# Performance work log

Measured on AMD Instinct MI355X. Metric: run time of the kernel, lower is better.

The kernel has to match this reference:

```python
import jax, jax.numpy as jnp
import numpy as np

T, HID, H, KV, D = 2048, 2048, 16, 8, 128
EPS = 1e-6
THETA = 10000.0


def setup_inputs() -> dict:
    key = jax.random.key(0)
    ks = jax.random.split(key, 6)
    positions = jnp.arange(T, dtype=jnp.int64 if jax.config.jax_enable_x64 else jnp.int32)
    hidden_states = jax.random.normal(ks[0], (T, HID), dtype=jnp.float32)
    scale = 0.02
    Wq = jax.random.normal(ks[1], (HID, H * 2 * D), dtype=jnp.float32) * scale
    Wk = jax.random.normal(ks[2], (HID, KV * D), dtype=jnp.float32) * scale
    Wv = jax.random.normal(ks[3], (HID, KV * D), dtype=jnp.float32) * scale
    Wo = jax.random.normal(ks[4], (H * D, HID), dtype=jnp.float32) * scale
    q_norm_w = jnp.zeros((D,), dtype=jnp.float32)  # torch init: zeros, applied as (1+w)
    k_norm_w = jnp.zeros((D,), dtype=jnp.float32)
    return {"positions": positions, "hidden_states": hidden_states, "Wq": Wq,
            "Wk": Wk, "Wv": Wv, "Wo": Wo, "q_norm_w": q_norm_w, "k_norm_w": k_norm_w}


def _rms_norm(x, w):
    # fp32 RMSNorm with (1 + weight) scaling, per last dim
    xf = x.astype(jnp.float32)
    inv = jax.lax.rsqrt(jnp.mean(xf * xf, axis=-1, keepdims=True) + EPS)
    return (xf * inv * (1.0 + w.astype(jnp.float32))).astype(x.dtype)


def _rope(x, positions):
    # neox-style rotary over full head_dim; x: (T, heads, D)
    half = D // 2
    inv_freq = 1.0 / (THETA ** (jnp.arange(0, half, dtype=jnp.float32) / half))
    freqs = positions.astype(jnp.float32)[:, None] * inv_freq  # (T, half)
    cos = jnp.cos(freqs)[:, None, :]  # (T,1,half)
    sin = jnp.sin(freqs)[:, None, :]
    x1, x2 = x[..., :half], x[..., half:]
    return jnp.concatenate([x1 * cos - x2 * sin, x2 * cos + x1 * sin], axis=-1)


def reference(positions, hidden_states, Wq, Wk, Wv, Wo, q_norm_w, k_norm_w):
    scaling = D ** -0.5
    qg = (hidden_states @ Wq).reshape(T, H, 2 * D)
    q, gate = qg[..., :D], qg[..., D:]              # (T,H,D) each
    k = (hidden_states @ Wk).reshape(T, KV, D)
    v = (hidden_states @ Wv).reshape(T, KV, D)
    q = _rms_norm(q, q_norm_w)
    k = _rms_norm(k, k_norm_w)
    q = _rope(q, positions)
    k = _rope(k, positions)
    # GQA: repeat kv heads
    rep = H // KV
    k = jnp.repeat(k, rep, axis=1)                   # (T,H,D)
    v = jnp.repeat(v, rep, axis=1)
    scores = jnp.einsum('thd,shd->hts', q, k) * scaling  # (H,T,T)
    causal = positions[:, None] >= positions[None, :]     # (T,T)
    scores = jnp.where(causal[None], scores, jnp.finfo(scores.dtype).min)
    probs = jax.nn.softmax(scores, axis=-1)
    o = jnp.einsum('hts,shd->thd', probs, v).reshape(T, H * D)
    o = o * jax.nn.sigmoid(gate.reshape(T, H * D))
    return o @ Wo
```

## Files before the change

kernel.cpp:

```cpp
#include <hip/hip_runtime.h>
#include <stdint.h>
#include <math.h>

#define T_SEQ 2048
#define HID   2048
#define NH    16
#define NKV   8
#define DH    128

typedef __bf16 bf16x8 __attribute__((ext_vector_type(8)));
typedef float  f32x4  __attribute__((ext_vector_type(4)));

__device__ __forceinline__ ushort f2bf(float f) {
  uint32_t u = __float_as_uint(f);
  u += 0x7FFF + ((u >> 16) & 1);
  return (ushort)(u >> 16);
}
__device__ __forceinline__ ushort f2bf_rz(float f) {
  return (ushort)(__float_as_uint(f) >> 16);
}
__device__ __forceinline__ float bf2f(ushort u) {
  return __uint_as_float(((uint32_t)u) << 16);
}
__device__ __forceinline__ void gld16(const void* g, void* l) {
  __builtin_amdgcn_global_load_lds(
      (const __attribute__((address_space(1))) uint32_t*)g,
      (__attribute__((address_space(3))) uint32_t*)l, 16, 0, 0);
}

__global__ __launch_bounds__(256) void prep_kernel(
    const float* __restrict__ hs, const float* __restrict__ Wq,
    const float* __restrict__ Wk, const float* __restrict__ Wv,
    const float* __restrict__ Wo, ushort* __restrict__ hs16,
    ushort* __restrict__ Wqt, ushort* __restrict__ Wkt,
    ushort* __restrict__ Wvt, ushort* __restrict__ Wot) {
  int bid = blockIdx.x;
  if (bid < 4096) {
    int i = (bid * 256 + threadIdx.x) * 4;
    float4 v = *(const float4*)(hs + i);
    ushort4 o = {f2bf(v.x), f2bf(v.y), f2bf(v.z), f2bf(v.w)};
    *(ushort4*)(hs16 + i) = o;
    return;
  }
  bid -= 4096;
  const float* src; ushort* dst; int N, bi, bj;
  if (bid < 2048)      { src = Wq; dst = Wqt; N = 4096; bj = bid & 63; bi = bid >> 6; }
  else if (bid < 2560) { bid -= 2048; src = Wk; dst = Wkt; N = 1024; bj = bid & 15; bi = bid >> 4; }
  else if (bid < 3072) { bid -= 2560; src = Wv; dst = Wvt; N = 1024; bj = bid & 15; bi = bid >> 4; }
  else                 { bid -= 3072; src = Wo; dst = Wot; N = 2048; bj = bid & 31; bi = bid >> 5; }
  __shared__ float tile[64][65];
  const int r = threadIdx.x >> 2, cg = (threadIdx.x & 3) * 16;
  const float* sp = src + (size_t)(bi * 64 + r) * N + bj * 64 + cg;
#pragma unroll
  for (int p = 0; p < 4; ++p) {
    float4 v = *(const float4*)(sp + p * 4);
    tile[r][cg + p * 4 + 0] = v.x; tile[r][cg + p * 4 + 1] = v.y;
    tile[r][cg + p * 4 + 2] = v.z; tile[r][cg + p * 4 + 3] = v.w;
  }
  __syncthreads();
  ushort* dp = dst + (size_t)(bj * 64 + r) * HID + bi * 64 + cg;
#pragma unroll
  for (int p = 0; p < 2; ++p) {
    union { uint4 v; ushort u[8]; } o;
#pragma unroll
    for (int j = 0; j < 8; ++j) o.u[j] = f2bf(tile[cg + p * 8 + j][r]);
    *(uint4*)(dp + p * 8) = o.v;
  }
}

template <int MI>
__device__ __forceinline__ void gemm_loop(
    const ushort* __restrict__ A, const ushort* __restrict__ Bt,
    int K, int m0, int n0, ushort* As, ushort* Bs, f32x4 (*acc)[4]) {
  const int tid = threadIdx.x, lane = tid & 63, w = tid >> 6;
  const int quad = lane >> 4, l15 = lane & 15;
  const int wm = (w >> 1) * (MI * 16), wn = (w & 1) * 64;
  const int srow = tid >> 2, sch = tid & 3;
  for (int k0 = 0; k0 < K; k0 += 32) {
    __syncthreads();
#pragma unroll
    for (int p = 0; p < MI / 2; ++p) {
      int row = p * 64 + srow;
      int gch = sch ^ ((row >> 1) & 3);
      gld16(A + (size_t)(m0 + row) * K + k0 + gch * 8,
            As + (p * 256 + w * 64) * 8);
    }
#pragma unroll
    for (int p = 0; p < 2; ++p) {
      int row = p * 64 + srow;
      int gch = sch ^ ((row >> 1) & 3);
      gld16(Bt + (size_t)(n0 + row) * K + k0 + gch * 8,
            Bs + (p * 256 + w * 64) * 8);
    }
    __syncthreads();
    bf16x8 af[MI], bfr[4];
#pragma unroll
    for (int mi = 0; mi < MI; ++mi) {
      int row = wm + mi * 16 + l15;
      int pch = quad ^ ((row >> 1) & 3);
      af[mi] = *(const bf16x8*)(As + row * 32 + pch * 8);
    }
#pragma unroll
    for (int ni = 0; ni < 4; ++ni) {
      int row = wn + ni * 16 + l15;
      int pch = quad ^ ((row >> 1) & 3);
      bfr[ni] = *(const bf16x8*)(Bs + row * 32 + pch * 8);
    }
#pragma unroll
    for (int mi = 0; mi < MI; ++mi)
#pragma unroll
      for (int ni = 0; ni < 4; ++ni)
        acc[mi][ni] = __builtin_amdgcn_mfma_f32_16x16x32_bf16(
            af[mi], bfr[ni], acc[mi][ni], 0, 0, 0);
  }
}


__device__ __forceinline__ void stage_half(const ushort* __restrict__ X,
                                           int Ksrc, int rowg0, int k0,
                                           ushort* lbase) {
  const int tid = threadIdx.x;
  const int rl = tid >> 3, ch = tid & 7, w = tid >> 6;
  const int gch = ch ^ (rl & 7);
#pragma unroll
  for (int p = 0; p < 2; ++p)
    gld16(X + (size_t)(rowg0 + p * 64 + rl) * Ksrc + k0 + gch * 8,
          lbase + p * 4096 + w * 512);
}

__device__ __forceinline__ void load_a(const ushort* base, int wr, int quad,
                                       int l15, bf16x8 af[4][2]) {
  const int sw = l15 & 7;
#pragma unroll
  for (int mi = 0; mi < 4; ++mi) {
    const ushort* rp = base + (wr * 64 + mi * 16 + l15) * 64;
#pragma unroll
    for (int ks = 0; ks < 2; ++ks)
      af[mi][ks] = *(const bf16x8*)(rp + ((ks * 4 + quad) ^ sw) * 8);
  }
}
__device__ __forceinline__ void load_b(const ushort* base, int wc, int quad,
                                       int l15, bf16x8 bq[2][2]) {
  const int sw = l15 & 7;
#pragma unroll
  for (int ni = 0; ni < 2; ++ni) {
    const ushort* rp = base + (wc * 32 + ni * 16 + l15) * 64;
#pragma unroll
    for (int ks = 0; ks < 2; ++ks)
      bq[ni][ks] = *(const bf16x8*)(rp + ((ks * 4 + quad) ^ sw) * 8);
  }
}
__device__ __forceinline__ void mfma_quad(const bf16x8 af[4][2],
                                          const bf16x8 bq[2][2],
                                          f32x4 acc[8][4], int mh, int nh) {
#pragma unroll
  for (int ks = 0; ks < 2; ++ks)
#pragma unroll
    for (int mi = 0; mi < 4; ++mi)
#pragma unroll
      for (int ni = 0; ni < 2; ++ni)
        acc[mh * 4 + mi][nh * 2 + ni] =
            __builtin_amdgcn_mfma_f32_16x16x32_bf16(
                af[mi][ks], bq[ni][ks], acc[mh * 4 + mi][nh * 2 + ni], 0, 0, 0);
}

#define PHASE_MID()                                     \
  __builtin_amdgcn_s_barrier();                         \
  asm volatile("s_waitcnt lgkmcnt(0)" ::: "memory");    \
  __builtin_amdgcn_sched_barrier(0)

__global__ __launch_bounds__(512, 2) void gemm_qkv256(
    const ushort* __restrict__ hs16, const ushort* __restrict__ Wqt,
    const ushort* __restrict__ Wkt, const ushort* __restrict__ Wvt,
    ushort* __restrict__ q16, ushort* __restrict__ gate16,
    ushort* __restrict__ k16, ushort* __restrict__ v16t) {
  __shared__ ushort As[2][2][8192];
  __shared__ ushort Bs[2][2][8192];

  const int b = blockIdx.x;
  const ushort* A; const ushort* Bt; int m0, n0, kind;
  if (b < 128)      { A = hs16; Bt = Wqt; m0 = (b >> 4) << 8; n0 = (b & 15) << 8; kind = 0; }
  else if (b < 160) { int f = b - 128; A = hs16; Bt = Wkt; m0 = (f >> 2) << 8; n0 = (f & 3) << 8; kind = 1; }
  else              { int f = b - 160; A = Wvt; Bt = hs16; m0 = (f >> 3) << 8; n0 = (f & 7) << 8; kind = 2; }

  const int tid = threadIdx.x, lane = tid & 63;
  const int quad = lane >> 4, l15 = lane & 15;
  const int wid = tid >> 6, wr = wid >> 2, wc = wid & 3;

  f32x4 acc[8][4];
#pragma unroll
  for (int i = 0; i < 8; ++i)
#pragma unroll
    for (int j = 0; j < 4; ++j) acc[i][j] = (f32x4){0.f, 0.f, 0.f, 0.f};

  constexpr int K = HID;
  constexpr int NKT = K / 64;

  stage_half(A,  K, m0,        0, &As[0][0][0]);
  stage_half(A,  K, m0 + 128,  0, &As[0][1][0]);
  stage_half(Bt, K, n0,        0, &Bs[0][0][0]);
  stage_half(Bt, K, n0 + 128,  0, &Bs[0][1][0]);
  stage_half(A,  K, m0,       64, &As[1][0][0]);
  stage_half(Bt, K, n0 + 128, 64, &Bs[1][1][0]);
  asm volatile("s_waitcnt vmcnt(4)" ::: "memory");
  __builtin_amdgcn_s_barrier();

  bf16x8 af[4][2], bq0[2][2], bq1[2][2];

#pragma unroll 1
  for (int t = 0; t < NKT; ++t) {
    const int buf = t & 1, nbuf = buf ^ 1;
    const ushort* pA0 = &As[buf][0][0];
    const ushort* pA1 = &As[buf][1][0];
    const ushort* pB0 = &Bs[buf][0][0];
    const ushort* pB1 = &Bs[buf][1][0];
    const int kt1 = (t + 1) * 64, kt2 = (t + 2) * 64;

    load_a(pA0, wr, quad, l15, af);
    load_b(pB0, wc, quad, l15, bq0);
    if (t + 1 < NKT) stage_half(Bt, K, n0, kt1, &Bs[nbuf][0][0]);
    PHASE_MID();
    __builtin_amdgcn_s_setprio(1);
    mfma_quad(af, bq0, acc, 0, 0);
    __builtin_amdgcn_s_setprio(0);
    __builtin_amdgcn_s_barrier();

    load_b(pB1, wc, quad, l15, bq1);
    if (t + 1 < NKT) stage_half(A, K, m0 + 128, kt1, &As[nbuf][1][0]);
    PHASE_MID();
    __builtin_amdgcn_s_setprio(1);
    mfma_quad(af, bq1, acc, 0, 1);
    __builtin_amdgcn_s_setprio(0);
    __builtin_amdgcn_s_barrier();

    load_a(pA1, wr, quad, l15, af);
    if (t + 2 < NKT) stage_half(A, K, m0, kt2, &As[buf][0][0]);
    PHASE_MID();
    __builtin_amdgcn_s_setprio(1);
    mfma_quad(af, bq1, acc, 1, 1);
    __builtin_amdgcn_s_setprio(0);
    __builtin_amdgcn_s_barrier();

    load_b(pB0, wc, quad, l15, bq0);
    if (t + 2 < NKT) stage_half(Bt, K, n0 + 128, kt2, &Bs[buf][1][0]);
    PHASE_MID();
    __builtin_amdgcn_s_setprio(1);
    mfma_quad(af, bq0, acc, 1, 0);
    __builtin_amdgcn_s_setprio(0);
    if (t + 2 < NKT) asm volatile("s_waitcnt vmcnt(4)" ::: "memory");
    else             asm volatile("s_waitcnt vmcnt(0)" ::: "memory");
    __builtin_amdgcn_s_barrier();
  }

  const int head = n0 >> 8;
#pragma unroll
  for (int mh = 0; mh < 2; ++mh)
#pragma unroll
    for (int mi = 0; mi < 4; ++mi)
#pragma unroll
      for (int nh = 0; nh < 2; ++nh)
#pragma unroll
        for (int ni = 0; ni < 2; ++ni)
#pragma unroll
          for (int r = 0; r < 4; ++r) {
            const int row = m0 + mh * 128 + wr * 64 + mi * 16 + quad * 4 + r;
            const int ic = wc * 32 + ni * 16 + l15;
            const ushort v = f2bf(acc[mh * 4 + mi][nh * 2 + ni][r]);
            if (kind == 0) {
              ushort* dst = nh ? gate16 : q16;
              dst[((size_t)row * NH + head) * DH + ic] = v;
            } else if (kind == 1) {
              k16[(size_t)row * 1024 + n0 + nh * 128 + ic] = v;
            } else {
              v16t[(size_t)row * T_SEQ + n0 + nh * 128 + ic] = v;
            }
          }
}

__global__ __launch_bounds__(256) void gemm_out(
    const ushort* __restrict__ ob16, const ushort* __restrict__ Wot,
    float* __restrict__ out) {
  __shared__ ushort As[64 * 32];
  __shared__ ushort Bs[128 * 32];
  f32x4 acc[2][4];
#pragma unroll
  for (int i = 0; i < 2; ++i)
#pragma unroll
    for (int j = 0; j < 4; ++j) acc[i][j] = (f32x4){0.f, 0.f, 0.f, 0.f};
  const int b = blockIdx.x;
  const int m0 = (b >> 4) * 64, n0 = (b & 15) * 128;
  gemm_loop<2>(ob16, Wot, HID, m0, n0, As, Bs, acc);
  const int lane = threadIdx.x & 63, w = threadIdx.x >> 6;
  const int quad = lane >> 4, l15 = lane & 15;
  const int wm = (w >> 1) * 32, wn = (w & 1) * 64;
#pragma unroll
  for (int mi = 0; mi < 2; ++mi)
#pragma unroll
    for (int ni = 0; ni < 4; ++ni)
#pragma unroll
      for (int r = 0; r < 4; ++r) {
        int row = m0 + wm + mi * 16 + quad * 4 + r;
        int col = n0 + wn + ni * 16 + l15;
        out[(size_t)row * HID + col] = acc[mi][ni][r];
      }
}

__global__ __launch_bounds__(128) void norm_qk(
    ushort* __restrict__ q16, ushort* __restrict__ k16,
    const int* __restrict__ positions, const float* __restrict__ qw,
    const float* __restrict__ kw) {
  const int t = blockIdx.x, hh = blockIdx.y, d = threadIdx.x;
  ushort* x; const float* wgt;
  if (hh < NH) { x = q16 + ((size_t)t * NH + hh) * DH; wgt = qw; }
  else         { x = k16 + ((size_t)t * NKV + (hh - NH)) * DH; wgt = kw; }
  float v = bf2f(x[d]);
  float ss = v * v;
#pragma unroll
  for (int off = 32; off >= 1; off >>= 1) ss += __shfl_xor(ss, off, 64);
  __shared__ float red[2];
  if ((d & 63) == 0) red[d >> 6] = ss;
  __syncthreads();
  float mean = (red[0] + red[1]) * (1.0f / 128.0f);
  float xn = v * rsqrtf(mean + 1e-6f) * (1.0f + wgt[d]);
  __shared__ float sh[128];
  sh[d] = xn;
  __syncthreads();
  if (d < 64) {
    float pos = (float)positions[t];
    float rev = pos * exp2f((float)d * -0.20762050593045233f) *
                0.15915494309189535f;
    float fr = rev - floorf(rev);
    float s = __builtin_amdgcn_sinf(fr);
    float c = __builtin_amdgcn_cosf(fr);
    float x1 = sh[d], x2 = sh[d + 64];
    x[d]      = f2bf(x1 * c - x2 * s);
    x[d + 64] = f2bf(x2 * c + x1 * s);
  }
}

__global__ __launch_bounds__(256) void attn_mfma(
    const ushort* __restrict__ q16, const ushort* __restrict__ k16,
    const ushort* __restrict__ v16t, const float* __restrict__ qnw,
    const float* __restrict__ knw, ushort* __restrict__ Op0,
    ushort* __restrict__ Op1, ushort* __restrict__ Op2,
    float* __restrict__ lpart) {
  const int pb = blockIdx.x, h = blockIdx.y, s = blockIdx.z, kvh = h >> 1;
  const int tid = threadIdx.x, lane = tid & 63, w = tid >> 6;
  const int quad = lane >> 4, l15 = lane & 15;

  __shared__ ushort Ks[64 * 128];
  __shared__ ushort Vs[144 * 64];
  __shared__ ushort Ps[4][16][72];

  for (int i = tid; i < 16 * 64; i += 256) {
    int row = 128 + (i >> 6), col = i & 63;
    Vs[row * 64 + col] = (row == 128) ? (ushort)0x3F80 : (ushort)0;
  }

  __shared__ float s8[8];
  __shared__ float bshare;
  {
    float mq = 0.f, mk = 0.f;
    if (tid < 128) { mq = fabsf(1.f + qnw[tid]); mk = fabsf(1.f + knw[tid]); }
#pragma unroll
    for (int off = 32; off >= 1; off >>= 1) {
      mq = fmaxf(mq, __shfl_xor(mq, off, 64));
      mk = fmaxf(mk, __shfl_xor(mk, off, 64));
    }
    if (lane == 0) { s8[w * 2] = mq; s8[w * 2 + 1] = mk; }
    __syncthreads();
    if (tid == 0) {
      float MQ = fmaxf(s8[0], s8[2]), MK = fmaxf(s8[1], s8[3]);
      bshare = 16.3217f * MQ * MK * 1.02f + 0.1f;
    }
    __syncthreads();
  }
  const float B = bshare;
  const float CSC = 0.08838834764831845f * 1.44269504088896f;

#pragma unroll 1
  for (int sel = 0; sel < 2; ++sel) {
    const int qt = sel ? (31 - pb) : pb;
    const int q0 = qt * 64;
    const int ntl = (qt >= s) ? ((qt - s) / 3 + 1) : 0;

    bf16x8 qf[4];
    const ushort* qbase = q16 + ((size_t)(q0 + w * 16 + l15) * NH + h) * DH;
#pragma unroll
    for (int ks = 0; ks < 4; ++ks)
      qf[ks] = *(const bf16x8*)(qbase + ks * 32 + quad * 8);

    f32x4 oacc[9];
#pragma unroll
    for (int i = 0; i < 9; ++i) oacc[i] = (f32x4){0.f, 0.f, 0.f, 0.f};

#pragma unroll 1
    for (int it = 0; it < ntl; ++it) {
      const int kt = s + 3 * it;
      const int kt0 = kt * 64;
      __syncthreads();
#pragma unroll
      for (int p = 0; p < 4; ++p) {
        int row = p * 16 + (tid >> 4), ch = tid & 15;
        int gch = ch ^ (row & 15);
        gld16(k16 + ((size_t)(kt0 + row) * NKV + kvh) * DH + gch * 8,
              Ks + (p * 256 + w * 64) * 8);
      }
#pragma unroll
      for (int p = 0; p < 4; ++p) {
        int row = p * 32 + (tid >> 3), ch = tid & 7;
        int gch = ch ^ (row & 7);
        gld16(v16t + (size_t)(kvh * DH + row) * T_SEQ + kt0 + gch * 8,
              Vs + (p * 256 + w * 64) * 8);
      }
      __syncthreads();

      f32x4 sacc[4];
#pragma unroll
      for (int ni = 0; ni < 4; ++ni) sacc[ni] = (f32x4){0.f, 0.f, 0.f, 0.f};
#pragma unroll
      for (int ks = 0; ks < 4; ++ks)
#pragma unroll
        for (int ni = 0; ni < 4; ++ni) {
          int row = ni * 16 + l15;
          int pch = (ks * 4 + quad) ^ (row & 15);
          bf16x8 kf = *(const bf16x8*)(Ks + row * 128 + pch * 8);
          sacc[ni] = __builtin_amdgcn_mfma_f32_16x16x32_bf16(
              qf[ks], kf, sacc[ni], 0, 0, 0);
        }

      const bool diag = (kt == qt);
#pragma unroll
      for (int ni = 0; ni < 4; ++ni) {
        int key = kt0 + ni * 16 + l15;
#pragma unroll
        for (int r = 0; r < 4; ++r) {
          float arg = fmaf(sacc[ni][r], CSC, -B);
          float pv;
          if (diag) {
            int q = q0 + w * 16 + quad * 4 + r;
            pv = (key <= q) ? exp2f(arg) : 0.f;
          } else {
            pv = exp2f(arg);
          }
          Ps[w][quad * 4 + r][ni * 16 + l15] = f2bf_rz(pv);
        }
      }

#pragma unroll
      for (int ks2 = 0; ks2 < 2; ++ks2) {
        bf16x8 pf = *(const bf16x8*)(&Ps[w][l15][ks2 * 32 + quad * 8]);
#pragma unroll
        for (int ni = 0; ni < 9; ++ni) {
          int row = ni * 16 + l15;
          int pch = (ks2 * 4 + quad) ^ (row & 7);
          bf16x8 vf = *(const bf16x8*)(Vs + row * 64 + pch * 8);
          oacc[ni] = __builtin_amdgcn_mfma_f32_16x16x32_bf16(
              pf, vf, oacc[ni], 0, 0, 0);
        }
      }
    }

    ushort* Op = (s == 0) ? Op0 : (s == 1) ? Op1 : Op2;
#pragma unroll
    for (int ni = 0; ni < 8; ++ni) {
      int d = ni * 16 + l15;
#pragma unroll
      for (int r = 0; r < 4; ++r) {
        int q = q0 + w * 16 + quad * 4 + r;
        Op[((size_t)h * T_SEQ + q) * DH + d] = f2bf(oacc[ni][r]);
      }
    }
    if (l15 == 0) {
#pragma unroll
      for (int r = 0; r < 4; ++r) {
        int q = q0 + w * 16 + quad * 4 + r;
        lpart[(size_t)s * (NH * T_SEQ) + h * T_SEQ + q] = oacc[8][r];
      }
    }
  }
}

__global__ __launch_bounds__(256) void combine_kernel(
    const ushort* __restrict__ Op0, const ushort* __restrict__ Op1,
    const ushort* __restrict__ Op2, const float* __restrict__ lpart,
    const ushort* __restrict__ gate16, ushort* __restrict__ ob16) {
  const int t = blockIdx.x, tid = threadIdx.x;
  const int h = tid >> 4, d0 = (tid & 15) * 8;
  const int NT = NH * T_SEQ;
  const float l = lpart[h * T_SEQ + t] + lpart[NT + h * T_SEQ + t] +
                  lpart[2 * NT + h * T_SEQ + t];
  const float inv = 1.0f / l;
  const size_t po = ((size_t)h * T_SEQ + t) * DH + d0;
  ushort4 a0 = *(const ushort4*)(Op0 + po);
  ushort4 a1 = *(const ushort4*)(Op0 + po + 4);
  ushort4 b0 = *(const ushort4*)(Op1 + po);
  ushort4 b1 = *(const ushort4*)(Op1 + po + 4);
  ushort4 c0 = *(const ushort4*)(Op2 + po);
  ushort4 c1 = *(const ushort4*)(Op2 + po + 4);
  const ushort* gp = gate16 + (size_t)t * (NH * DH) + h * DH + d0;
  ushort4 g0 = *(const ushort4*)(gp);
  ushort4 g1 = *(const ushort4*)(gp + 4);
  float oa[8] = {bf2f(a0.x), bf2f(a0.y), bf2f(a0.z), bf2f(a0.w),
                 bf2f(a1.x), bf2f(a1.y), bf2f(a1.z), bf2f(a1.w)};
  float ob[8] = {bf2f(b0.x), bf2f(b0.y), bf2f(b0.z), bf2f(b0.w),
                 bf2f(b1.x), bf2f(b1.y), bf2f(b1.z), bf2f(b1.w)};
  float oc[8] = {bf2f(c0.x), bf2f(c0.y), bf2f(c0.z), bf2f(c0.w),
                 bf2f(c1.x), bf2f(c1.y), bf2f(c1.z), bf2f(c1.w)};
  float gg[8] = {bf2f(g0.x), bf2f(g0.y), bf2f(g0.z), bf2f(g0.w),
                 bf2f(g1.x), bf2f(g1.y), bf2f(g1.z), bf2f(g1.w)};
  ushort r[8];
#pragma unroll
  for (int i = 0; i < 8; ++i) {
    float o = (oa[i] + ob[i] + oc[i]) * inv;
    o = o / (1.0f + exp2f(-gg[i] * 1.44269504088896f));
    r[i] = f2bf(o);
  }
  ushort* op = ob16 + (size_t)t * (NH * DH) + h * DH + d0;
  *(ushort4*)(op)     = (ushort4){r[0], r[1], r[2], r[3]};
  *(ushort4*)(op + 4) = (ushort4){r[4], r[5], r[6], r[7]};
}

extern "C" void kernel_launch(void* const* d_in, const int* in_sizes, int n_in,
                              void* d_out, int out_size, void* d_ws, size_t ws_size,
                              hipStream_t stream) {
  const int*   positions = (const int*)d_in[0];
  const float* hs  = (const float*)d_in[1];
  const float* Wq  = (const float*)d_in[2];
  const float* Wk  = (const float*)d_in[3];
  const float* Wv  = (const float*)d_in[4];
  const float* Wo  = (const float*)d_in[5];
  const float* qnw = (const float*)d_in[6];
  const float* knw = (const float*)d_in[7];
  float* out = (float*)d_out;

  const size_t MB = 1 << 20;
  uint8_t* ws = (uint8_t*)d_ws;
  ushort* hs16  = (ushort*)(ws + 0);
  ushort* Op0   = (ushort*)(ws + 0);
  ushort* Wqt   = (ushort*)(ws + 8 * MB);
  ushort* Op1   = (ushort*)(ws + 8 * MB);
  ushort* Op2   = (ushort*)(ws + 16 * MB);
  ushort* Wkt   = (ushort*)(ws + 24 * MB);
  ushort* ob16  = (ushort*)(ws + 24 * MB);
  ushort* Wvt   = (ushort*)(ws + 28 * MB);
  ushort* v16t  = (ushort*)(ws + 32 * MB);
  ushort* k16   = (ushort*)(ws + 36 * MB);
  ushort* q16   = (ushort*)(ws + 40 * MB);
  ushort* gate16= (ushort*)(ws + 48 * MB);
  ushort* Wot   = (ushort*)(ws + 56 * MB);
  float*  lpart = (float*)d_out;

  prep_kernel<<<8192, 256, 0, stream>>>(hs, Wq, Wk, Wv, Wo,
                                        hs16, Wqt, Wkt, Wvt, Wot);
  gemm_qkv256<<<192, 512, 0, stream>>>(hs16, Wqt, Wkt, Wvt,
                                       q16, gate16, k16, v16t);
  norm_qk<<<dim3(T_SEQ, NH + NKV), 128, 0, stream>>>(q16, k16, positions,
                                                     qnw, knw);
  attn_mfma<<<dim3(16, NH, 3), 256, 0, stream>>>(q16, k16, v16t, qnw, knw,
                                                 Op0, Op1, Op2, lpart);
  combine_kernel<<<T_SEQ, 256, 0, stream>>>(Op0, Op1, Op2, lpart, gate16, ob16);
  gemm_out<<<512, 256, 0, stream>>>(ob16, Wot, out);
}
```

Baseline: 283.7 us.

## Software-pipeline LDS fragment reads one phase ahead in QKV GEMM

Restructures the QKV GEMM main loop into an unrolled even/odd schedule. Shared-memory fragment reads for the next phase are issued before the current MFMA phase, so MFMA no longer waits on a full lgkmcnt(0) drain, and global prefetch runs deeper with finer vmcnt waits. Extra fragment registers (af0/af1, bqA/bqB) raise register pressure and risk spills at 2 blocks per CU, and the hand-counted waitcnt values must match the issued loads exactly.

```diff
diff --git a/kernel.cpp b/kernel.cpp
--- a/kernel.cpp
+++ b/kernel.cpp
@@ -128,8 +128,8 @@
           lbase + p * 4096 + w * 512);
 }
 
-__device__ __forceinline__ void load_a(const ushort* base, int wr, int quad,
-                                       int l15, bf16x8 af[4][2]) {
+__device__ __forceinline__ void rd_a(const ushort* base, int wr, int quad,
+                                     int l15, bf16x8 (&af)[4][2]) {
   const int sw = l15 & 7;
 #pragma unroll
   for (int mi = 0; mi < 4; ++mi) {
@@ -139,8 +139,8 @@
       af[mi][ks] = *(const bf16x8*)(rp + ((ks * 4 + quad) ^ sw) * 8);
   }
 }
-__device__ __forceinline__ void load_b(const ushort* base, int wc, int quad,
-                                       int l15, bf16x8 bq[2][2]) {
+__device__ __forceinline__ void rd_b(const ushort* base, int wc, int quad,
+                                     int l15, bf16x8 (&bq)[2][2]) {
   const int sw = l15 & 7;
 #pragma unroll
   for (int ni = 0; ni < 2; ++ni) {
@@ -150,9 +150,9 @@
       bq[ni][ks] = *(const bf16x8*)(rp + ((ks * 4 + quad) ^ sw) * 8);
   }
 }
-__device__ __forceinline__ void mfma_quad(const bf16x8 af[4][2],
-                                          const bf16x8 bq[2][2],
-                                          f32x4 acc[8][4], int mh, int nh) {
+__device__ __forceinline__ void mm(const bf16x8 (&af)[4][2],
+                                   const bf16x8 (&bq)[2][2],
+                                   f32x4 (&acc)[8][4], int mh, int nh) {
 #pragma unroll
   for (int ks = 0; ks < 2; ++ks)
 #pragma unroll
@@ -164,10 +164,39 @@
                 af[mi][ks], bq[ni][ks], acc[mh * 4 + mi][nh * 2 + ni], 0, 0, 0);
 }
 
-#define PHASE_MID()                                     \
-  __builtin_amdgcn_s_barrier();                         \
-  asm volatile("s_waitcnt lgkmcnt(0)" ::: "memory");    \
-  __builtin_amdgcn_sched_barrier(0)
+#define PH(RD, STG, LGKM, MM_, VM)                                   \
+  do {                                                               \
+    RD;                                                              \
+    STG;                                                             \
+    __builtin_amdgcn_s_barrier();                                    \
+    asm volatile("s_waitcnt lgkmcnt(" LGKM ")" ::: "memory");        \
+    __builtin_amdgcn_sched_barrier(0);                               \
+    __builtin_amdgcn_s_setprio(1);                                   \
+    MM_;                                                             \
+    __builtin_amdgcn_s_setprio(0);                                   \
+    asm volatile("s_waitcnt vmcnt(" VM ")" ::: "memory");            \
+    __builtin_amdgcn_s_barrier();                                    \
+  } while (0)
+
+#define EVEN_T(S1, S2, S3, S4, V1, V2, V3, V4)                        \
+  PH((rd_b(&Bs[0][1][0], wc, quad, l15, bq1)), S1, "4",               \
+     (mm(af0, bqA, acc, 0, 0)), V1);                                  \
+  PH((rd_a(&As[0][1][0], wr, quad, l15, af1)), S2, "8",               \
+     (mm(af0, bq1, acc, 0, 1)), V2);                                  \
+  PH((rd_a(&As[1][0][0], wr, quad, l15, af0)), S3, "8",               \
+     (mm(af1, bq1, acc, 1, 1)), V3);                                  \
+  PH((rd_b(&Bs[1][0][0], wc, quad, l15, bqB)), S4, "4",               \
+     (mm(af1, bqA, acc, 1, 0)), V4)
+
+#define ODD_T(S1, S2, S3, S4, V1, V2, V3, V4)                         \
+  PH((rd_b(&Bs[1][1][0], wc, quad, l15, bq1)), S1, "4",               \
+     (mm(af0, bqB, acc, 0, 0)), V1);                                  \
+  PH((rd_a(&As[1][1][0], wr, quad, l15, af1)), S2, "8",               \
+     (mm(af0, bq1, acc, 0, 1)), V2);                                  \
+  PH((rd_a(&As[0][0][0], wr, quad, l15, af0)), S3, "8",               \
+     (mm(af1, bq1, acc, 1, 1)), V3);                                  \
+  PH((rd_b(&Bs[0][0][0], wc, quad, l15, bqA)), S4, "4",               \
+     (mm(af1, bqB, acc, 1, 0)), V4)
 
 __global__ __launch_bounds__(512, 2) void gemm_qkv256(
     const ushort* __restrict__ hs16, const ushort* __restrict__ Wqt,
@@ -194,63 +223,44 @@
     for (int j = 0; j < 4; ++j) acc[i][j] = (f32x4){0.f, 0.f, 0.f, 0.f};
 
   constexpr int K = HID;
-  constexpr int NKT = K / 64;
-
-  stage_half(A,  K, m0,        0, &As[0][0][0]);
-  stage_half(A,  K, m0 + 128,  0, &As[0][1][0]);
-  stage_half(Bt, K, n0,        0, &Bs[0][0][0]);
-  stage_half(Bt, K, n0 + 128,  0, &Bs[0][1][0]);
-  stage_half(A,  K, m0,       64, &As[1][0][0]);
-  stage_half(Bt, K, n0 + 128, 64, &Bs[1][1][0]);
-  asm volatile("s_waitcnt vmcnt(4)" ::: "memory");
+
+  bf16x8 af0[4][2], af1[4][2], bq1[2][2], bqA[2][2], bqB[2][2];
+
+  stage_half(A,  K, m0,        0,  &As[0][0][0]);
+  stage_half(Bt, K, n0,        0,  &Bs[0][0][0]);
+  stage_half(Bt, K, n0 + 128,  0,  &Bs[0][1][0]);
+  stage_half(A,  K, m0 + 128,  0,  &As[0][1][0]);
+  stage_half(A,  K, m0,        64, &As[1][0][0]);
+  stage_half(Bt, K, n0,        64, &Bs[1][0][0]);
+  stage_half(Bt, K, n0 + 128,  64, &Bs[1][1][0]);
+  asm volatile("s_waitcnt vmcnt(6)" ::: "memory");
   __builtin_amdgcn_s_barrier();
-
-  bf16x8 af[4][2], bq0[2][2], bq1[2][2];
+  rd_a(&As[0][0][0], wr, quad, l15, af0);
+  rd_b(&Bs[0][0][0], wc, quad, l15, bqA);
 
 #pragma unroll 1
-  for (int t = 0; t < NKT; ++t) {
-    const int buf = t & 1, nbuf = buf ^ 1;
-    const ushort* pA0 = &As[buf][0][0];
-    const ushort* pA1 = &As[buf][1][0];
-    const ushort* pB0 = &Bs[buf][0][0];
-    const ushort* pB1 = &Bs[buf][1][0];
-    const int kt1 = (t + 1) * 64, kt2 = (t + 2) * 64;
-
-    load_a(pA0, wr, quad, l15, af);
-    load_b(pB0, wc, quad, l15, bq0);
-    if (t + 1 < NKT) stage_half(Bt, K, n0, kt1, &Bs[nbuf][0][0]);
-    PHASE_MID();
-    __builtin_amdgcn_s_setprio(1);
-    mfma_quad(af, bq0, acc, 0, 0);
-    __builtin_amdgcn_s_setprio(0);
-    __builtin_amdgcn_s_barrier();
-
-    load_b(pB1, wc, quad, l15, bq1);
-    if (t + 1 < NKT) stage_half(A, K, m0 + 128, kt1, &As[nbuf][1][0]);
-    PHASE_MID();
-    __builtin_amdgcn_s_setprio(1);
-    mfma_quad(af, bq1, acc, 0, 1);
-    __builtin_amdgcn_s_setprio(0);
-    __builtin_amdgcn_s_barrier();
-
-    load_a(pA1, wr, quad, l15, af);
-    if (t + 2 < NKT) stage_half(A, K, m0, kt2, &As[buf][0][0]);
-    PHASE_MID();
-    __builtin_amdgcn_s_setprio(1);
-    mfma_quad(af, bq1, acc, 1, 1);
-    __builtin_amdgcn_s_setprio(0);
-    __builtin_amdgcn_s_barrier();
-
-    load_b(pB0, wc, quad, l15, bq0);
-    if (t + 2 < NKT) stage_half(Bt, K, n0 + 128, kt2, &Bs[buf][1][0]);
-    PHASE_MID();
-    __builtin_amdgcn_s_setprio(1);
-    mfma_quad(af, bq0, acc, 1, 0);
-    __builtin_amdgcn_s_setprio(0);
-    if (t + 2 < NKT) asm volatile("s_waitcnt vmcnt(4)" ::: "memory");
-    else             asm volatile("s_waitcnt vmcnt(0)" ::: "memory");
-    __builtin_amdgcn_s_barrier();
-  }
+  for (int e = 0; e < 30; e += 2) {
+    EVEN_T((stage_half(A,  K, m0 + 128, (e + 1) * 64, &As[1][1][0])),
+           (stage_half(A,  K, m0,       (e + 2) * 64, &As[0][0][0])),
+           (stage_half(Bt, K, n0,       (e + 2) * 64, &Bs[0][0][0])),
+           (stage_half(Bt, K, n0 + 128, (e + 2) * 64, &Bs[0][1][0])),
+           "8", "8", "8", "8");
+    ODD_T((stage_half(A,  K, m0 + 128, (e + 2) * 64, &As[0][1][0])),
+          (stage_half(A,  K, m0,       (e + 3) * 64, &As[1][0][0])),
+          (stage_half(Bt, K, n0,       (e + 3) * 64, &Bs[1][0][0])),
+          (stage_half(Bt, K, n0 + 128, (e + 3) * 64, &Bs[1][1][0])),
+          "8", "8", "8", "8");
+  }
+
+  EVEN_T((stage_half(A, K, m0 + 128, 31 * 64, &As[1][1][0])),
+         ((void)0), ((void)0), ((void)0),
+         "8", "6", "4", "2");
+  PH((rd_b(&Bs[1][1][0], wc, quad, l15, bq1)), ((void)0), "4",
+     (mm(af0, bqB, acc, 0, 0)), "0");
+  PH((rd_a(&As[1][1][0], wr, quad, l15, af1)), ((void)0), "8",
+     (mm(af0, bq1, acc, 0, 1)), "0");
+  PH(((void)0), ((void)0), "0", (mm(af1, bq1, acc, 1, 1)), "0");
+  PH(((void)0), ((void)0), "0", (mm(af1, bqB, acc, 1, 0)), "0");
 
   const int head = n0 >> 8;
 #pragma unroll
```

Result: slower. 298.3 us (+5.2%).
